# Kernel tuning notes

Measured on AMD Instinct MI355X. Metric: run time of the kernel, lower is better.

## Reference

```python
import jax, jax.numpy as jnp
import numpy as np

S, B, H = 4096, 64, 256
D = 2.0
SIGMA = D / 2.0


def setup_inputs() -> dict:
    key = jax.random.key(0)
    ks = jax.random.split(key, 7)
    return {
        "e": jax.random.normal(ks[0], (S, B, H), dtype=jnp.float32),
        "d": jax.random.normal(ks[1], (1, B, H), dtype=jnp.float32),
        "W_a": jax.random.normal(ks[2], (H, H), dtype=jnp.float32) / np.sqrt(H),
        "W_p": jax.random.normal(ks[3], (H, H), dtype=jnp.float32) / np.sqrt(H),
        "v_p": jax.random.normal(ks[4], (H, 1), dtype=jnp.float32) / np.sqrt(H),
        "lin_w": jax.random.normal(ks[5], (H, 2 * H), dtype=jnp.float32) / np.sqrt(2 * H),
        "lin_b": jax.random.normal(ks[6], (H,), dtype=jnp.float32) * 0.01,
    }


def reference(e, d, W_a, W_p, v_p, lin_w, lin_b):
    s = e.shape[0]
    # alignment: scores over source positions, softmax along S (dim 0 in torch)
    scores = jnp.sum((d @ W_a) * e, axis=2)          # [S, B]
    a = jax.nn.softmax(scores, axis=0)               # [S, B]
    # predictive position gating (Luong local-p attention)
    h = jnp.tanh(d[0] @ W_p)                         # [B, H]
    p_center = jax.nn.sigmoid((h @ v_p)[:, 0])[None, :] * s   # [1, B]
    pos = jnp.arange(s, dtype=e.dtype)[:, None]      # [S, 1]
    diff = p_center - pos                            # [S, B]
    mask = (jnp.abs(diff) <= D).astype(e.dtype)
    p = jnp.exp(-(diff * diff) / (2.0 * SIGMA * SIGMA)) * mask  # [S, B]
    w = a * p                                        # [S, B]
    context = jnp.einsum('sbh,sb->bh', e, w)[None]   # [1, B, H]
    x = jnp.concatenate([context, d], axis=2)        # [1, B, 2H]
    out = jax.nn.relu(x @ lin_w.T + lin_b)           # dropout = identity (eval)
    return out, w
```

## Files before the change

### kernel.cpp

```cpp
#include <hip/hip_runtime.h>
#include <math.h>

constexpr int S_ = 4096;
constexpr int B_ = 64;
constexpr int H_ = 256;


__global__ __launch_bounds__(1024) void k1_prep(const float* __restrict__ d,
                                                const float* __restrict__ W_a,
                                                const float* __restrict__ W_p,
                                                const float* __restrict__ v_p,
                                                float* __restrict__ dW,
                                                float* __restrict__ pc) {
  int b = blockIdx.x;
  int t = threadIdx.x;
  int h = t & 255;
  int kc = t >> 8;
  const float* db = d + b * H_;
  float acc_a = 0.f, acc_p = 0.f;
#pragma unroll 8
  for (int k = kc * 64; k < kc * 64 + 64; ++k) {
    float dv = db[k];
    acc_a = fmaf(dv, W_a[k * H_ + h], acc_a);
    acc_p = fmaf(dv, W_p[k * H_ + h], acc_p);
  }
  __shared__ float part[4][256];
  part[kc][h] = acc_a;
  __syncthreads();
  float dwa = 0.f;
  if (t < 256) dwa = part[0][t] + part[1][t] + part[2][t] + part[3][t];
  __syncthreads();
  part[kc][h] = acc_p;
  __syncthreads();
  __shared__ float red[256];
  if (t < 256) {
    dW[b * H_ + t] = dwa;
    float dwp = part[0][t] + part[1][t] + part[2][t] + part[3][t];
    red[t] = tanhf(dwp) * v_p[t];
  }
  __syncthreads();
  for (int st = 128; st > 0; st >>= 1) {
    if (t < st) red[t] += red[t + st];
    __syncthreads();
  }
  if (t == 0) pc[b] = (float)S_ / (1.f + expf(-red[0]));
}

__global__ __launch_bounds__(256) void k2_scores(const float* __restrict__ e,
                                                 const float* __restrict__ dW,
                                                 float* __restrict__ scores) {
  int t = threadIdx.x;
  int wave = t >> 6;
  int lane = t & 63;
  int bl = lane >> 2;
  int sub = lane & 3;
  int b = wave * 16 + bl;
  int s0 = blockIdx.x * 4;

  const float4* dW4 = (const float4*)(dW + b * H_);
  float4 wreg[16];
#pragma unroll
  for (int j = 0; j < 16; ++j) wreg[j] = dW4[sub + 4 * j];

  float sc[4];
#pragma unroll
  for (int r = 0; r < 4; ++r) {
    const float4* erow = (const float4*)(e + ((size_t)(s0 + r) * B_ + b) * H_);
    float acc = 0.f;
#pragma unroll
    for (int half = 0; half < 2; ++half) {
      float4 ev[8];
#pragma unroll
      for (int j = 0; j < 8; ++j) ev[j] = erow[sub + 4 * (half * 8 + j)];
#pragma unroll
      for (int j = 0; j < 8; ++j) {
        const float4 wv = wreg[half * 8 + j];
        acc = fmaf(ev[j].x, wv.x, fmaf(ev[j].y, wv.y,
              fmaf(ev[j].z, wv.z, fmaf(ev[j].w, wv.w, acc))));
      }
    }
    acc += __shfl_xor(acc, 1, 64);
    acc += __shfl_xor(acc, 2, 64);
    sc[r] = acc;
  }

  __shared__ float tile[4][64];
  if (sub == 0) {
#pragma unroll
    for (int r = 0; r < 4; ++r) tile[r][b] = sc[r];
  }
  __syncthreads();
  int b_out = t >> 2, r = t & 3;
  scores[b_out * S_ + s0 + r] = tile[r][b_out];
}

__global__ __launch_bounds__(1024) void kF(const float* __restrict__ scores,
                                           const float* __restrict__ pc,
                                           const float* __restrict__ e,
                                           const float* __restrict__ d,
                                           const float* __restrict__ lin_w,
                                           const float* __restrict__ lin_b,
                                           float* __restrict__ out,
                                           float* __restrict__ w_out) {
  int b = blockIdx.x;
  int t = threadIdx.x;
  const float* sc = scores + b * S_;
  float v[4];
  float lm = -INFINITY;
#pragma unroll
  for (int k = 0; k < 4; ++k) {
    v[k] = sc[t + k * 1024];
    lm = fmaxf(lm, v[k]);
  }
  __shared__ float red[1024];
  red[t] = lm;
  __syncthreads();
  for (int st = 512; st > 0; st >>= 1) {
    if (t < st) red[t] = fmaxf(red[t], red[t + st]);
    __syncthreads();
  }
  float mb = red[0];
  __syncthreads();
  float ls = 0.f;
#pragma unroll
  for (int k = 0; k < 4; ++k) ls += expf(v[k] - mb);
  red[t] = ls;
  __syncthreads();
  for (int st = 512; st > 0; st >>= 1) {
    if (t < st) red[t] += red[t + st];
    __syncthreads();
  }
  float inv_l = 1.f / red[0];
  float pcb = pc[b];
#pragma unroll
  for (int k = 0; k < 4; ++k) {
    int s = t + k * 1024;
    float diff = pcb - (float)s;
    float p = (fabsf(diff) <= 2.f) ? expf(-0.5f * diff * diff) : 0.f;
    w_out[(size_t)s * B_ + b] = expf(v[k] - mb) * inv_l * p;
  }
  __shared__ float x[512];
  if (t < 256) {
    int s0 = max(0, (int)ceilf(pcb - 2.f));
    int s1 = min(S_ - 1, (int)floorf(pcb + 2.f));
    float ctx = 0.f;
    for (int s = s0; s <= s1; ++s) {
      float diff = pcb - (float)s;
      float wv = expf(sc[s] - mb) * inv_l * expf(-0.5f * diff * diff);
      ctx = fmaf(wv, e[((size_t)s * B_ + b) * H_ + t], ctx);
    }
    x[t] = ctx;
  } else if (t < 512) {
    x[t] = d[b * H_ + (t - 256)];
  }
  __syncthreads();
  int h = t >> 2, part = t & 3;
  const float4* lw = (const float4*)(lin_w + h * 2 * H_) + part * 32;
  const float4* xv = (const float4*)x + part * 32;
  float acc = 0.f;
#pragma unroll 8
  for (int k = 0; k < 32; ++k) {
    float4 a4 = lw[k];
    float4 b4 = xv[k];
    acc += a4.x * b4.x + a4.y * b4.y + a4.z * b4.z + a4.w * b4.w;
  }
  red[t] = acc;
  __syncthreads();
  if (t < 256) {
    float r = red[4 * t] + red[4 * t + 1] + red[4 * t + 2] + red[4 * t + 3] + lin_b[t];
    out[b * H_ + t] = fmaxf(r, 0.f);
  }
}

extern "C" void kernel_launch(void* const* d_in, const int* in_sizes, int n_in,
                              void* d_out, int out_size, void* d_ws, size_t ws_size,
                              hipStream_t stream) {
  const float* e     = (const float*)d_in[0];
  const float* d     = (const float*)d_in[1];
  const float* W_a   = (const float*)d_in[2];
  const float* W_p   = (const float*)d_in[3];
  const float* v_p   = (const float*)d_in[4];
  const float* lin_w = (const float*)d_in[5];
  const float* lin_b = (const float*)d_in[6];

  float* out   = (float*)d_out;
  float* w_out = out + B_ * H_;

  float* ws     = (float*)d_ws;
  float* dW     = ws;
  float* pc     = ws + 16384;
  float* scores = ws + 16448;

  k1_prep<<<B_, 1024, 0, stream>>>(d, W_a, W_p, v_p, dW, pc);
  k2_scores<<<S_ / 4, 256, 0, stream>>>(e, dW, scores);
  kF<<<B_, 1024, 0, stream>>>(scores, pc, e, d, lin_w, lin_b, out, w_out);
}
```

Baseline: 80.06 us.

## Split final stage into stats and wide output kernels, widen prep grid

The prep kernel now runs 256 blocks of 256 threads, one per batch and quarter of H, instead of 64 blocks of 1024. Each block writes a partial v_p dot product, and the partials are combined later. The fused softmax/output kernel is split in two: a 64-block stats kernel computes the max, the sum and the p_center, then a 320-block kernel writes w_out coalesced across 256 blocks while 64 blocks compute context and the linear layer. This spreads the strided w_out writes and the prep work over more CUs, at the cost of one extra kernel launch and a second read of the scores.

```diff
diff --git a/kernel.cpp b/kernel.cpp
--- a/kernel.cpp
+++ b/kernel.cpp
@@ -6,47 +6,43 @@
 constexpr int H_ = 256;
 
 
-__global__ __launch_bounds__(1024) void k1_prep(const float* __restrict__ d,
-                                                const float* __restrict__ W_a,
-                                                const float* __restrict__ W_p,
-                                                const float* __restrict__ v_p,
-                                                float* __restrict__ dW,
-                                                float* __restrict__ pc) {
-  int b = blockIdx.x;
-  int t = threadIdx.x;
-  int h = t & 255;
-  int kc = t >> 8;
+__global__ __launch_bounds__(256) void kA_prep(const float* __restrict__ d,
+                                               const float* __restrict__ W_a,
+                                               const float* __restrict__ W_p,
+                                               const float* __restrict__ v_p,
+                                               float* __restrict__ dW,
+                                               float* __restrict__ hppart) {
+  const int b = blockIdx.x >> 2;
+  const int hc = blockIdx.x & 3;
+  const int t = threadIdx.x;
+  const int hl = t & 63;
+  const int h = hc * 64 + hl;
+  const int kc = t >> 6;
   const float* db = d + b * H_;
-  float acc_a = 0.f, acc_p = 0.f;
+  float aa = 0.f, ap = 0.f;
 #pragma unroll 8
   for (int k = kc * 64; k < kc * 64 + 64; ++k) {
     float dv = db[k];
-    acc_a = fmaf(dv, W_a[k * H_ + h], acc_a);
-    acc_p = fmaf(dv, W_p[k * H_ + h], acc_p);
-  }
-  __shared__ float part[4][256];
-  part[kc][h] = acc_a;
-  __syncthreads();
-  float dwa = 0.f;
-  if (t < 256) dwa = part[0][t] + part[1][t] + part[2][t] + part[3][t];
-  __syncthreads();
-  part[kc][h] = acc_p;
-  __syncthreads();
-  __shared__ float red[256];
-  if (t < 256) {
-    dW[b * H_ + t] = dwa;
-    float dwp = part[0][t] + part[1][t] + part[2][t] + part[3][t];
-    red[t] = tanhf(dwp) * v_p[t];
-  }
-  __syncthreads();
-  for (int st = 128; st > 0; st >>= 1) {
-    if (t < st) red[t] += red[t + st];
-    __syncthreads();
-  }
-  if (t == 0) pc[b] = (float)S_ / (1.f + expf(-red[0]));
-}
-
-__global__ __launch_bounds__(256) void k2_scores(const float* __restrict__ e,
+    aa = fmaf(dv, W_a[k * H_ + h], aa);
+    ap = fmaf(dv, W_p[k * H_ + h], ap);
+  }
+  __shared__ float redA[256];
+  __shared__ float redB[256];
+  redA[t] = aa;
+  redB[t] = ap;
+  __syncthreads();
+  if (t < 64) {
+    float sa = redA[t] + redA[t + 64] + redA[t + 128] + redA[t + 192];
+    float sp = redB[t] + redB[t + 64] + redB[t + 128] + redB[t + 192];
+    dW[b * H_ + hc * 64 + t] = sa;
+    float val = tanhf(sp) * v_p[hc * 64 + t];
+#pragma unroll
+    for (int off = 32; off > 0; off >>= 1) val += __shfl_xor(val, off, 64);
+    if (t == 0) hppart[blockIdx.x] = val;
+  }
+}
+
+__global__ __launch_bounds__(256) void kB_scores(const float* __restrict__ e,
                                                  const float* __restrict__ dW,
                                                  float* __restrict__ scores) {
   int t = threadIdx.x;
@@ -94,69 +90,90 @@
   scores[b_out * S_ + s0 + r] = tile[r][b_out];
 }
 
-__global__ __launch_bounds__(1024) void kF(const float* __restrict__ scores,
-                                           const float* __restrict__ pc,
-                                           const float* __restrict__ e,
-                                           const float* __restrict__ d,
-                                           const float* __restrict__ lin_w,
-                                           const float* __restrict__ lin_b,
-                                           float* __restrict__ out,
-                                           float* __restrict__ w_out) {
-  int b = blockIdx.x;
-  int t = threadIdx.x;
+__global__ __launch_bounds__(256) void kC_stats(const float* __restrict__ scores,
+                                                const float* __restrict__ hppart,
+                                                float* __restrict__ Mv,
+                                                float* __restrict__ Lv,
+                                                float* __restrict__ pcv) {
+  const int b = blockIdx.x;
+  const int t = threadIdx.x;
   const float* sc = scores + b * S_;
-  float v[4];
+  float v[16];
   float lm = -INFINITY;
 #pragma unroll
-  for (int k = 0; k < 4; ++k) {
-    v[k] = sc[t + k * 1024];
+  for (int k = 0; k < 16; ++k) {
+    v[k] = sc[t + k * 256];
     lm = fmaxf(lm, v[k]);
   }
-  __shared__ float red[1024];
+  __shared__ float red[256];
   red[t] = lm;
   __syncthreads();
-  for (int st = 512; st > 0; st >>= 1) {
+  for (int st = 128; st > 0; st >>= 1) {
     if (t < st) red[t] = fmaxf(red[t], red[t + st]);
     __syncthreads();
   }
-  float mb = red[0];
+  const float M = red[0];
   __syncthreads();
   float ls = 0.f;
 #pragma unroll
-  for (int k = 0; k < 4; ++k) ls += expf(v[k] - mb);
+  for (int k = 0; k < 16; ++k) ls += expf(v[k] - M);
   red[t] = ls;
   __syncthreads();
-  for (int st = 512; st > 0; st >>= 1) {
+  for (int st = 128; st > 0; st >>= 1) {
     if (t < st) red[t] += red[t + st];
     __syncthreads();
   }
-  float inv_l = 1.f / red[0];
-  float pcb = pc[b];
-#pragma unroll
-  for (int k = 0; k < 4; ++k) {
-    int s = t + k * 1024;
-    float diff = pcb - (float)s;
-    float p = (fabsf(diff) <= 2.f) ? expf(-0.5f * diff * diff) : 0.f;
-    w_out[(size_t)s * B_ + b] = expf(v[k] - mb) * inv_l * p;
-  }
-  __shared__ float x[512];
+  if (t == 0) {
+    Mv[b] = M;
+    Lv[b] = red[0];
+    float hp = hppart[4 * b] + hppart[4 * b + 1] + hppart[4 * b + 2] + hppart[4 * b + 3];
+    pcv[b] = (float)S_ / (1.f + expf(-hp));
+  }
+}
+
+__global__ __launch_bounds__(1024) void kD_out(const float* __restrict__ scores,
+                                               const float* __restrict__ Mv,
+                                               const float* __restrict__ Lv,
+                                               const float* __restrict__ pcv,
+                                               const float* __restrict__ e,
+                                               const float* __restrict__ d,
+                                               const float* __restrict__ lin_w,
+                                               const float* __restrict__ lin_b,
+                                               float* __restrict__ out,
+                                               float* __restrict__ w_out) {
+  const int t = threadIdx.x;
+  if (blockIdx.x < 256) {
+    const int s = blockIdx.x * 16 + (t >> 6);
+    const int b = t & 63;
+    const float diff = pcv[b] - (float)s;
+    float w = 0.f;
+    if (fabsf(diff) <= 2.f)
+      w = expf(scores[b * S_ + s] - Mv[b]) / Lv[b] * expf(-0.5f * diff * diff);
+    w_out[(size_t)s * B_ + b] = w;
+    return;
+  }
+  const int b = blockIdx.x - 256;
+  __shared__ float xbuf[512];
+  __shared__ float red[1024];
   if (t < 256) {
+    const float pcb = pcv[b];
+    const float M = Mv[b];
+    const float invL = 1.f / Lv[b];
     int s0 = max(0, (int)ceilf(pcb - 2.f));
     int s1 = min(S_ - 1, (int)floorf(pcb + 2.f));
     float ctx = 0.f;
     for (int s = s0; s <= s1; ++s) {
       float diff = pcb - (float)s;
-      float wv = expf(sc[s] - mb) * inv_l * expf(-0.5f * diff * diff);
+      float wv = expf(scores[b * S_ + s] - M) * invL * expf(-0.5f * diff * diff);
       ctx = fmaf(wv, e[((size_t)s * B_ + b) * H_ + t], ctx);
     }
-    x[t] = ctx;
-  } else if (t < 512) {
-    x[t] = d[b * H_ + (t - 256)];
-  }
-  __syncthreads();
-  int h = t >> 2, part = t & 3;
+    xbuf[t] = ctx;
+    xbuf[256 + t] = d[b * H_ + t];
+  }
+  __syncthreads();
+  const int h = t >> 2, part = t & 3;
   const float4* lw = (const float4*)(lin_w + h * 2 * H_) + part * 32;
-  const float4* xv = (const float4*)x + part * 32;
+  const float4* xv = (const float4*)xbuf + part * 32;
   float acc = 0.f;
 #pragma unroll 8
   for (int k = 0; k < 32; ++k) {
@@ -176,7 +193,7 @@
                               void* d_out, int out_size, void* d_ws, size_t ws_size,
                               hipStream_t stream) {
   const float* e     = (const float*)d_in[0];
-  const float* d     = (const float*)d_in[1];
+  const float* dd    = (const float*)d_in[1];
   const float* W_a   = (const float*)d_in[2];
   const float* W_p   = (const float*)d_in[3];
   const float* v_p   = (const float*)d_in[4];
@@ -188,10 +205,14 @@
 
   float* ws     = (float*)d_ws;
   float* dW     = ws;
-  float* pc     = ws + 16384;
-  float* scores = ws + 16448;
-
-  k1_prep<<<B_, 1024, 0, stream>>>(d, W_a, W_p, v_p, dW, pc);
-  k2_scores<<<S_ / 4, 256, 0, stream>>>(e, dW, scores);
-  kF<<<B_, 1024, 0, stream>>>(scores, pc, e, d, lin_w, lin_b, out, w_out);
-}
+  float* hppart = ws + 16384;
+  float* pcv    = ws + 16640;
+  float* Mv     = ws + 16704;
+  float* Lv     = ws + 16768;
+  float* scores = ws + 16832;
+
+  kA_prep<<<256, 256, 0, stream>>>(dd, W_a, W_p, v_p, dW, hppart);
+  kB_scores<<<S_ / 4, 256, 0, stream>>>(e, dW, scores);
+  kC_stats<<<B_, 256, 0, stream>>>(scores, hppart, Mv, Lv, pcv);
+  kD_out<<<320, 1024, 0, stream>>>(scores, Mv, Lv, pcv, e, dd, lin_w, lin_b, out, w_out);
+}
```

Measured after the change: 74.91 us. 1.07x faster.
